# Optimization experiments

Measured on AMD Instinct MI355X. Metric: run time of the kernel, lower is better.

## Reference

```python
import jax, jax.numpy as jnp
import numpy as np

EPS_DIV = 1e-6    # safe_div clamp
EPS_NORM = 1e-12  # F.normalize eps
EPS_PD = 1e-6     # F.pairwise_distance eps (added to the difference)


def setup_inputs() -> dict:
    key = jax.random.key(0)
    k1, k2, k3 = jax.random.split(key, 3)
    B, N, D, C = 8, 2048, 512, 8192
    x = jax.random.normal(k1, (B, N, D), dtype=jnp.float32)
    W = jax.random.normal(k2, (D, D), dtype=jnp.float32) * (1.0 / np.sqrt(D))
    codebook = jax.random.normal(k3, (C, D), dtype=jnp.float32)
    return {"x": x, "W": W, "codebook": codebook}


def reference(x, W, codebook):
    sg = jax.lax.stop_gradient
    # implicit codebook = Linear(dim, dim, bias=False)(codebook)  -> codebook @ W^T
    imp = codebook @ W.T                                  # [C, D]

    lead = x.shape[:-1]
    D = x.shape[-1]
    xf = x.reshape(-1, D)                                 # [T, D]

    # nearest-neighbor search (no_grad in original): squared-dist argmin == cdist argmin
    d2 = (jnp.sum(xf * xf, axis=-1, keepdims=True)
          - 2.0 * (xf @ imp.T)
          + jnp.sum(imp * imp, axis=-1)[None, :])         # [T, C]
    indices = jnp.argmin(sg(d2), axis=-1)                 # [T]

    qf = imp[indices]                                     # [T, D] gather

    # commit loss: (pairwise_distance(x, q.detach())**2).mean(); torch adds eps to the diff
    diff = xf - sg(qf) + EPS_PD
    commit_loss = jnp.mean(jnp.sum(diff * diff, axis=-1))

    # rotation trick
    norm_x = jnp.linalg.norm(xf, axis=-1, keepdims=True)  # [T, 1]
    norm_q = jnp.linalg.norm(qf, axis=-1, keepdims=True)
    u = xf / jnp.maximum(norm_x, EPS_DIV)
    q = qf / jnp.maximum(norm_q, EPS_DIV)
    s = u + q
    w = sg(s / jnp.maximum(jnp.linalg.norm(s, axis=-1, keepdims=True), EPS_NORM))
    e = xf
    # e - 2 (e.w) w + 2 (e.u_sg) q_sg   (rank-1 products per row)
    rot = (e
           - 2.0 * jnp.sum(e * w, axis=-1, keepdims=True) * w
           + 2.0 * jnp.sum(e * sg(u), axis=-1, keepdims=True) * sg(q))
    quantized = rot * sg(norm_q / jnp.maximum(norm_x, EPS_DIV))

    quantized = quantized.reshape(*lead, D)
    indices = indices.reshape(*lead)
    return quantized, indices, commit_loss
```

## Files before the change

### kernel.cpp

```cpp
#include <hip/hip_runtime.h>
#include <cstdint>
#include <cstddef>

#define DD 512
#define TT 16384
#define CC 8192
#define RT 256
#define CT 128
#define NSPLIT (CC / CT)
#define EPS_DIV 1e-6f
#define EPS_NORM 1e-12f
#define EPS_PD 1e-6f

typedef _Float16 half8 __attribute__((ext_vector_type(8)));
typedef _Float16 half4 __attribute__((ext_vector_type(4)));
typedef float floatx4 __attribute__((ext_vector_type(4)));

#define GLDS16(g, l) __builtin_amdgcn_global_load_lds( \
    (const __attribute__((address_space(1))) void*)(g), \
    (__attribute__((address_space(3))) void*)(l), 16, 0, 0)

__global__ __launch_bounds__(256) void k_prep(
    const float* __restrict__ cb, const float* __restrict__ W,
    _Float16* __restrict__ cbs, _Float16* __restrict__ Ws) {
  const int b = blockIdx.x;
  const float* src;
  _Float16* dst;
  int row;
  if (b < CC / 2) {
    row = b * 2 + (threadIdx.x >> 7);
    src = cb; dst = cbs;
  } else {
    row = (b - CC / 2) * 2 + (threadIdx.x >> 7);
    src = W; dst = Ws;
  }
  const int col = (threadIdx.x & 127) * 4;
  float4 v = *(const float4*)(src + (size_t)row * DD + col);
  half4 h, l;
  h.x = (_Float16)v.x; l.x = (_Float16)(v.x - (float)h.x);
  h.y = (_Float16)v.y; l.y = (_Float16)(v.y - (float)h.y);
  h.z = (_Float16)v.z; l.z = (_Float16)(v.z - (float)h.z);
  h.w = (_Float16)v.w; l.w = (_Float16)(v.w - (float)h.w);
  *(half4*)(dst + (size_t)row * 1024 + col) = h;
  *(half4*)(dst + (size_t)row * 1024 + 512 + col) = l;
}

__global__ __launch_bounds__(256) void k_gemm_mfma(
    const _Float16* __restrict__ cbs, const _Float16* __restrict__ Ws,
    float* __restrict__ imp, _Float16* __restrict__ ih,
    float* __restrict__ cnp) {
  __shared__ __align__(16) char smem[65536];
  const int tid = threadIdx.x;
  const int w = tid >> 6, lane = tid & 63;
  const int quad = lane >> 4, l15 = lane & 15;
  const int wm = (w & 1) * 64, wn = (w >> 1) * 64;
  const int c0 = blockIdx.x * 128;
  const int n0 = blockIdx.y * 128;

  const int srow8 = lane >> 3;
  const int scol = ((lane & 7) ^ srow8) << 3;
  size_t arow[4], brow[4];
#pragma unroll
  for (int j = 0; j < 4; ++j) {
    arow[j] = (size_t)(c0 + j * 32 + w * 8 + srow8) * 1024 + scol;
    brow[j] = (size_t)(n0 + j * 32 + w * 8 + srow8) * 1024 + scol;
  }
  int aoff[4], boff[4];
#pragma unroll
  for (int i = 0; i < 4; ++i) {
    aoff[i] = ((wm + i * 16 + l15) * 64 + ((quad ^ (l15 & 7)) << 3)) * 2;
    boff[i] = ((wn + i * 16 + l15) * 64 + ((quad ^ (l15 & 7)) << 3)) * 2;
  }

  auto stage = [&](int buf, int ak, int bk) {
    char* ab = smem + buf * 32768;
    char* bb = ab + 16384;
#pragma unroll
    for (int j = 0; j < 4; ++j) {
      GLDS16(cbs + arow[j] + ak, (_Float16*)ab + (j * 32 + w * 8) * 64);
      GLDS16(Ws  + brow[j] + bk, (_Float16*)bb + (j * 32 + w * 8) * 64);
    }
  };

  floatx4 acc[4][4] = {};
  stage(0, 0, 0);
#pragma unroll 2
  for (int it = 0; it < 24; ++it) {
    __syncthreads();
    if (it < 23) {
      const int n = it + 1;
      const int p = n >> 3, kk = n & 7;
      const int ak = ((p == 2) ? 512 : 0) + kk * 64;
      const int bk = ((p == 1) ? 512 : 0) + kk * 64;
      stage(n & 1, ak, bk);
    }
    const char* ab = smem + (it & 1) * 32768;
    const char* bb = ab + 16384;
#pragma unroll
    for (int ks = 0; ks < 2; ++ks) {
      const int kx = ks * 64;
      half8 a[4], b[4];
#pragma unroll
      for (int mi = 0; mi < 4; ++mi)
        a[mi] = *(const half8*)(ab + (aoff[mi] ^ kx));
#pragma unroll
      for (int ni = 0; ni < 4; ++ni)
        b[ni] = *(const half8*)(bb + (boff[ni] ^ kx));
#pragma unroll
      for (int mi = 0; mi < 4; ++mi)
#pragma unroll
        for (int ni = 0; ni < 4; ++ni)
          acc[mi][ni] = __builtin_amdgcn_mfma_f32_16x16x32_f16(
              a[mi], b[ni], acc[mi][ni], 0, 0, 0);
    }
  }
  __syncthreads();
  float* Csh = (float*)smem;
#pragma unroll
  for (int mi = 0; mi < 4; ++mi)
#pragma unroll
    for (int r = 0; r < 4; ++r) {
      const int row = wm + mi * 16 + quad * 4 + r;
      const int key = (row & 7) << 2;
#pragma unroll
      for (int ni = 0; ni < 4; ++ni) {
        const int col = wn + ni * 16 + l15;
        Csh[row * 128 + (col ^ key)] = acc[mi][ni][r];
      }
    }
  __syncthreads();
#pragma unroll
  for (int i = 0; i < 16; ++i) {
    const int row = (tid >> 5) * 16 + i;
    const int col = (tid & 31) * 4;
    const int key = (row & 7) << 2;
    const float4 v = *(const float4*)&Csh[row * 128 + (col ^ key)];
    *(float4*)&imp[(size_t)(c0 + row) * DD + n0 + col] = v;
    half4 h;
    h.x = (_Float16)v.x; h.y = (_Float16)v.y;
    h.z = (_Float16)v.z; h.w = (_Float16)v.w;
    *(half4*)&ih[(size_t)(c0 + row) * DD + n0 + col] = h;
    float ss = v.x * v.x + v.y * v.y + v.z * v.z + v.w * v.w;
#pragma unroll
    for (int m = 1; m < 32; m <<= 1) ss += __shfl_xor(ss, m);
    if ((tid & 31) == 0) cnp[(size_t)(n0 >> 7) * CC + c0 + row] = ss;
  }
}

__global__ __launch_bounds__(256) void k_cast_cnorm(
    const float* __restrict__ x, _Float16* __restrict__ xh,
    const float* __restrict__ cnp, float* __restrict__ cnorm) {
  const int b = blockIdx.x;
  if (b < TT / 2) {
    const size_t base = (size_t)b * 1024 + threadIdx.x * 4;
    float4 v = *(const float4*)(x + base);
    half4 h;
    h.x = (_Float16)v.x; h.y = (_Float16)v.y;
    h.z = (_Float16)v.z; h.w = (_Float16)v.w;
    *(half4*)(xh + base) = h;
  } else {
    const int row = (b - TT / 2) * 256 + threadIdx.x;
    cnorm[row] = cnp[row] + cnp[CC + row] + cnp[2 * CC + row] + cnp[3 * CC + row];
  }
}

__global__ __launch_bounds__(256, 2) void k_dist_top2(
    const _Float16* __restrict__ xh, const _Float16* __restrict__ ih,
    const float* __restrict__ cnorm,
    float* __restrict__ bval, int* __restrict__ bidx) {
  __shared__ __align__(16) char smem[49152];
  const int tid = threadIdx.x;
  const int mw = tid >> 6, lane = tid & 63;
  const int quad = lane >> 4, l15 = lane & 15;
  const int r0 = blockIdx.x * RT;
  const int c0 = blockIdx.y * CT;

  const _Float16* gA = xh + (size_t)(r0 + tid) * DD;
  const _Float16* gB = ih + (size_t)(c0 + (tid & 127)) * DD + (tid >> 7) * 8;

  int aoff[4], boff[8];
#pragma unroll
  for (int mi = 0; mi < 4; ++mi)
    aoff[mi] = quad * 4096 + (mw * 64 + mi * 16 + l15) * 16;
#pragma unroll
  for (int ni = 0; ni < 8; ++ni)
    boff[ni] = quad * 2048 + (ni * 16 + l15) * 16;

  auto stage = [&](int s) {
    char* ab = smem + (s & 1) * 24576;
    char* bb = ab + 16384;
    const int k0 = s * 32;
#pragma unroll
    for (int r = 0; r < 4; ++r)
      GLDS16(gA + k0 + r * 8, ab + (r * 256 + mw * 64) * 16);
#pragma unroll
    for (int r = 0; r < 2; ++r)
      GLDS16(gB + k0 + r * 16, bb + (r * 256 + mw * 64) * 16);
  };

  floatx4 acc[4][8] = {};
  stage(0);
#pragma unroll 2
  for (int s = 0; s < 16; ++s) {
    __syncthreads();
    if (s < 15) stage(s + 1);
    const char* ab = smem + (s & 1) * 24576;
    const char* bb = ab + 16384;
    half8 a[4], b[8];
#pragma unroll
    for (int mi = 0; mi < 4; ++mi) a[mi] = *(const half8*)(ab + aoff[mi]);
#pragma unroll
    for (int ni = 0; ni < 8; ++ni) b[ni] = *(const half8*)(bb + boff[ni]);
#pragma unroll
    for (int mi = 0; mi < 4; ++mi)
#pragma unroll
      for (int ni = 0; ni < 8; ++ni)
        acc[mi][ni] = __builtin_amdgcn_mfma_f32_16x16x32_f16(
            a[mi], b[ni], acc[mi][ni], 0, 0, 0);
  }
  float cn[8];
#pragma unroll
  for (int ni = 0; ni < 8; ++ni) cn[ni] = cnorm[c0 + ni * 16 + l15];
  float best[16];
  int bsti[16];
#pragma unroll
  for (int mi = 0; mi < 4; ++mi)
#pragma unroll
    for (int r = 0; r < 4; ++r) {
      const int sl = mi * 4 + r;
      best[sl] = 3.4e38f; bsti[sl] = 0;
#pragma unroll
      for (int ni = 0; ni < 8; ++ni) {
        const float v = fmaf(-2.0f, acc[mi][ni][r], cn[ni]);
        if (v < best[sl]) { best[sl] = v; bsti[sl] = c0 + ni * 16 + l15; }
      }
    }
  __syncthreads();
  float* rv = (float*)smem;
  int* ri = (int*)(smem + 16384);
#pragma unroll
  for (int mi = 0; mi < 4; ++mi)
#pragma unroll
    for (int r = 0; r < 4; ++r) {
      const int rowl = mw * 64 + mi * 16 + quad * 4 + r;
      rv[rowl * 16 + l15] = best[mi * 4 + r];
      ri[rowl * 16 + l15] = bsti[mi * 4 + r];
    }
  __syncthreads();
  {
    const int row = tid;
    float v1 = 3.4e38f, v2 = 3.4e38f;
    int i1 = 0x7fffffff, i2 = 0x7fffffff;
#pragma unroll
    for (int t = 0; t < 16; ++t) {
      const float v = rv[row * 16 + t];
      const int i = ri[row * 16 + t];
      if (v < v1 || (v == v1 && i < i1)) {
        v2 = v1; i2 = i1; v1 = v; i1 = i;
      } else if (v < v2 || (v == v2 && i < i2)) {
        v2 = v; i2 = i;
      }
    }
    const size_t o = ((size_t)blockIdx.y * TT + r0 + row) * 2;
    bval[o] = v1; bval[o + 1] = v2;
    bidx[o] = i1; bidx[o + 1] = i2;
  }
}

__global__ __launch_bounds__(256) void k_epilogue(
    const float* __restrict__ x, const float* __restrict__ imp,
    const float* __restrict__ cnorm,
    const float* __restrict__ bval, const int* __restrict__ bidx,
    float* __restrict__ outq, float* __restrict__ outidx,
    float* __restrict__ rloss) {
  const int lane = threadIdx.x & 63;
  const int row = blockIdx.x * 4 + (threadIdx.x >> 6);
  const size_t o = ((size_t)lane * TT + row) * 2;
  float v1 = bval[o], v2 = bval[o + 1];
  int i1 = bidx[o], i2 = bidx[o + 1];
#pragma unroll
  for (int m = 1; m < 64; m <<= 1) {
    const float w1 = __shfl_xor(v1, m), w2 = __shfl_xor(v2, m);
    const int j1 = __shfl_xor(i1, m), j2 = __shfl_xor(i2, m);
    if (w1 < v1 || (w1 == v1 && j1 < i1)) {
      if (v1 < w2 || (v1 == w2 && i1 < j2)) { v2 = v1; i2 = i1; }
      else { v2 = w2; i2 = j2; }
      v1 = w1; i1 = j1;
    } else {
      if (w1 < v2 || (w1 == v2 && j1 < i2)) { v2 = w1; i2 = j1; }
    }
  }
  const float* xr = x + (size_t)row * DD + lane * 8;
  float e[8], qa[8], qb[8];
  *(float4*)&e[0] = *(const float4*)xr;
  *(float4*)&e[4] = *(const float4*)(xr + 4);
  const float* q1p = imp + (size_t)i1 * DD + lane * 8;
  const float* q2p = imp + (size_t)i2 * DD + lane * 8;
  *(float4*)&qa[0] = *(const float4*)q1p;
  *(float4*)&qa[4] = *(const float4*)(q1p + 4);
  *(float4*)&qb[0] = *(const float4*)q2p;
  *(float4*)&qb[4] = *(const float4*)(q2p + 4);
  float d1 = 0.f, d2 = 0.f;
#pragma unroll
  for (int k = 0; k < 8; ++k) {
    d1 = fmaf(e[k], qa[k], d1);
    d2 = fmaf(e[k], qb[k], d2);
  }
#pragma unroll
  for (int m = 1; m < 64; m <<= 1) {
    d1 += __shfl_xor(d1, m);
    d2 += __shfl_xor(d2, m);
  }
  const float s1 = fmaf(-2.0f, d1, cnorm[i1]);
  const float s2 = fmaf(-2.0f, d2, cnorm[i2]);
  const bool use2 = (s2 < s1) || (s2 == s1 && i2 < i1);
  const int idx = use2 ? i2 : i1;
  float q[8];
#pragma unroll
  for (int k = 0; k < 8; ++k) q[k] = use2 ? qb[k] : qa[k];

  float xx = 0.f, qq = 0.f, xq = 0.f, cl = 0.f;
#pragma unroll
  for (int k = 0; k < 8; ++k) {
    xx = fmaf(e[k], e[k], xx);
    qq = fmaf(q[k], q[k], qq);
    xq = fmaf(e[k], q[k], xq);
    float d = e[k] - q[k] + EPS_PD;
    cl = fmaf(d, d, cl);
  }
#pragma unroll
  for (int m = 1; m < 64; m <<= 1) {
    xx += __shfl_xor(xx, m);
    qq += __shfl_xor(qq, m);
    xq += __shfl_xor(xq, m);
    cl += __shfl_xor(cl, m);
  }
  const float nx = sqrtf(xx), nq = sqrtf(qq);
  const float dx = fmaxf(nx, EPS_DIV), dq = fmaxf(nq, EPS_DIV);
  const float uu = xx / (dx * dx);
  const float qq2 = qq / (dq * dq);
  const float uq = xq / (dx * dq);
  const float ss = uu + qq2 + 2.0f * uq;
  const float dn = fmaxf(sqrtf(ss), EPS_NORM);
  const float es = xx / dx + xq / dq;
  const float a = 2.0f * es / (dn * dn);
  const float b = 2.0f * (xx / dx);
  const float scale = nq / dx;

  float ov[8];
#pragma unroll
  for (int k = 0; k < 8; ++k) {
    const float qp = q[k] / dq;
    const float sk = e[k] / dx + qp;
    ov[k] = (e[k] - a * sk + b * qp) * scale;
  }
  float* op = outq + (size_t)row * DD + lane * 8;
  *(float4*)op = *(const float4*)&ov[0];
  *(float4*)(op + 4) = *(const float4*)&ov[4];
  if (lane == 0) {
    outidx[row] = (float)idx;
    rloss[row] = cl;
  }
}

__global__ __launch_bounds__(256) void k_loss_final(
    const float* __restrict__ rloss, float* __restrict__ out) {
  __shared__ double red[256];
  const int tid = threadIdx.x;
  double s = 0.0;
  for (int i = tid; i < TT; i += 256) s += (double)rloss[i];
  red[tid] = s;
  __syncthreads();
  for (int st = 128; st > 0; st >>= 1) {
    if (tid < st) red[tid] += red[tid + st];
    __syncthreads();
  }
  if (tid == 0) out[0] = (float)(red[0] / (double)TT);
}

extern "C" void kernel_launch(void* const* d_in, const int* in_sizes, int n_in,
                              void* d_out, int out_size, void* d_ws, size_t ws_size,
                              hipStream_t stream) {
  const float* x  = (const float*)d_in[0];
  const float* W  = (const float*)d_in[1];
  const float* cb = (const float*)d_in[2];
  float* out = (float*)d_out;

  float* imp = (float*)d_ws;
  _Float16* ih = (_Float16*)(imp + (size_t)CC * DD);
  _Float16* cbs = ih + (size_t)CC * DD;
  _Float16* xh = cbs;
  _Float16* Ws = cbs + (size_t)CC * 1024;
  float* cnp   = (float*)(Ws + (size_t)DD * 1024);
  float* cnorm = cnp + 4 * CC;
  float* bval  = cnorm + CC;
  int*   bidx  = (int*)(bval + (size_t)NSPLIT * TT * 2);
  float* rloss = (float*)(bidx + (size_t)NSPLIT * TT * 2);

  float* out_q    = out;
  float* out_idx  = out + (size_t)TT * DD;
  float* out_loss = out_idx + TT;

  k_prep<<<CC / 2 + DD / 2, 256, 0, stream>>>(cb, W, cbs, Ws);
  k_gemm_mfma<<<dim3(CC / 128, DD / 128), 256, 0, stream>>>(cbs, Ws, imp, ih, cnp);
  k_cast_cnorm<<<TT / 2 + CC / 256, 256, 0, stream>>>(x, xh, cnp, cnorm);
  k_dist_top2<<<dim3(TT / RT, CC / CT), 256, 0, stream>>>(xh, ih, cnorm, bval, bidx);
  k_epilogue<<<TT / 4, 256, 0, stream>>>(x, imp, cnorm, bval, bidx, out_q, out_idx, rloss);
  k_loss_final<<<1, 256, 0, stream>>>(rloss, out_loss);
}
```

Baseline: 390.5 us.

## Use K-panel layout for fp16 operands and load MFMA fragments directly from global

```diff
diff --git a/kernel.cpp b/kernel.cpp
--- a/kernel.cpp
+++ b/kernel.cpp
@@ -22,32 +22,46 @@
 
 __global__ __launch_bounds__(256) void k_prep(
     const float* __restrict__ cb, const float* __restrict__ W,
-    _Float16* __restrict__ cbs, _Float16* __restrict__ Ws) {
+    const float* __restrict__ x,
+    _Float16* __restrict__ cbs, _Float16* __restrict__ Ws,
+    _Float16* __restrict__ xh_t) {
   const int b = blockIdx.x;
-  const float* src;
-  _Float16* dst;
-  int row;
-  if (b < CC / 2) {
-    row = b * 2 + (threadIdx.x >> 7);
-    src = cb; dst = cbs;
+  if (b < CC / 2 + DD / 2) {
+    const float* src;
+    _Float16* dst;
+    int row;
+    if (b < CC / 2) {
+      row = b * 2 + (threadIdx.x >> 7);
+      src = cb; dst = cbs;
+    } else {
+      row = (b - CC / 2) * 2 + (threadIdx.x >> 7);
+      src = W; dst = Ws;
+    }
+    const int col = (threadIdx.x & 127) * 4;
+    float4 v = *(const float4*)(src + (size_t)row * DD + col);
+    half4 h, l;
+    h.x = (_Float16)v.x; l.x = (_Float16)(v.x - (float)h.x);
+    h.y = (_Float16)v.y; l.y = (_Float16)(v.y - (float)h.y);
+    h.z = (_Float16)v.z; l.z = (_Float16)(v.z - (float)h.z);
+    h.w = (_Float16)v.w; l.w = (_Float16)(v.w - (float)h.w);
+    *(half4*)(dst + (size_t)row * 1024 + col) = h;
+    *(half4*)(dst + (size_t)row * 1024 + 512 + col) = l;
   } else {
-    row = (b - CC / 2) * 2 + (threadIdx.x >> 7);
-    src = W; dst = Ws;
-  }
-  const int col = (threadIdx.x & 127) * 4;
-  float4 v = *(const float4*)(src + (size_t)row * DD + col);
-  half4 h, l;
-  h.x = (_Float16)v.x; l.x = (_Float16)(v.x - (float)h.x);
-  h.y = (_Float16)v.y; l.y = (_Float16)(v.y - (float)h.y);
-  h.z = (_Float16)v.z; l.z = (_Float16)(v.z - (float)h.z);
-  h.w = (_Float16)v.w; l.w = (_Float16)(v.w - (float)h.w);
-  *(half4*)(dst + (size_t)row * 1024 + col) = h;
-  *(half4*)(dst + (size_t)row * 1024 + 512 + col) = l;
+    const int b2 = b - (CC / 2 + DD / 2);
+    const int row = b2 * 2 + (threadIdx.x >> 7);
+    const int col = (threadIdx.x & 127) * 4;
+    float4 v = *(const float4*)(x + (size_t)row * DD + col);
+    half4 h;
+    h.x = (_Float16)v.x; h.y = (_Float16)v.y;
+    h.z = (_Float16)v.z; h.w = (_Float16)v.w;
+    const int p = col >> 5, off = col & 31;
+    *(half4*)(xh_t + ((size_t)p * TT + row) * 32 + off) = h;
+  }
 }
 
 __global__ __launch_bounds__(256) void k_gemm_mfma(
     const _Float16* __restrict__ cbs, const _Float16* __restrict__ Ws,
-    float* __restrict__ imp, _Float16* __restrict__ ih,
+    float* __restrict__ imp, _Float16* __restrict__ ih_t,
     float* __restrict__ cnp) {
   __shared__ __align__(16) char smem[65536];
   const int tid = threadIdx.x;
@@ -139,7 +153,9 @@
     half4 h;
     h.x = (_Float16)v.x; h.y = (_Float16)v.y;
     h.z = (_Float16)v.z; h.w = (_Float16)v.w;
-    *(half4*)&ih[(size_t)(c0 + row) * DD + n0 + col] = h;
+    const int d = n0 + col;
+    const int p = d >> 5, off = d & 31;
+    *(half4*)(ih_t + ((size_t)p * CC + c0 + row) * 32 + off) = h;
     float ss = v.x * v.x + v.y * v.y + v.z * v.z + v.w * v.w;
 #pragma unroll
     for (int m = 1; m < 32; m <<= 1) ss += __shfl_xor(ss, m);
@@ -147,70 +163,38 @@
   }
 }
 
-__global__ __launch_bounds__(256) void k_cast_cnorm(
-    const float* __restrict__ x, _Float16* __restrict__ xh,
-    const float* __restrict__ cnp, float* __restrict__ cnorm) {
-  const int b = blockIdx.x;
-  if (b < TT / 2) {
-    const size_t base = (size_t)b * 1024 + threadIdx.x * 4;
-    float4 v = *(const float4*)(x + base);
-    half4 h;
-    h.x = (_Float16)v.x; h.y = (_Float16)v.y;
-    h.z = (_Float16)v.z; h.w = (_Float16)v.w;
-    *(half4*)(xh + base) = h;
-  } else {
-    const int row = (b - TT / 2) * 256 + threadIdx.x;
-    cnorm[row] = cnp[row] + cnp[CC + row] + cnp[2 * CC + row] + cnp[3 * CC + row];
-  }
-}
-
 __global__ __launch_bounds__(256, 2) void k_dist_top2(
-    const _Float16* __restrict__ xh, const _Float16* __restrict__ ih,
-    const float* __restrict__ cnorm,
+    const _Float16* __restrict__ xh_t, const _Float16* __restrict__ ih_t,
+    const float* __restrict__ cnp,
     float* __restrict__ bval, int* __restrict__ bidx) {
-  __shared__ __align__(16) char smem[49152];
+  __shared__ float rv[256 * 16];
+  __shared__ int   ri[256 * 16];
   const int tid = threadIdx.x;
   const int mw = tid >> 6, lane = tid & 63;
   const int quad = lane >> 4, l15 = lane & 15;
   const int r0 = blockIdx.x * RT;
   const int c0 = blockIdx.y * CT;
 
-  const _Float16* gA = xh + (size_t)(r0 + tid) * DD;
-  const _Float16* gB = ih + (size_t)(c0 + (tid & 127)) * DD + (tid >> 7) * 8;
-
-  int aoff[4], boff[8];
+  const char* pa = (const char*)xh_t;
+  const char* pb = (const char*)ih_t;
+  int voa[4], vob[8];
 #pragma unroll
   for (int mi = 0; mi < 4; ++mi)
-    aoff[mi] = quad * 4096 + (mw * 64 + mi * 16 + l15) * 16;
+    voa[mi] = ((r0 + mw * 64 + mi * 16 + l15) * 32 + quad * 8) * 2;
 #pragma unroll
   for (int ni = 0; ni < 8; ++ni)
-    boff[ni] = quad * 2048 + (ni * 16 + l15) * 16;
-
-  auto stage = [&](int s) {
-    char* ab = smem + (s & 1) * 24576;
-    char* bb = ab + 16384;
-    const int k0 = s * 32;
-#pragma unroll
-    for (int r = 0; r < 4; ++r)
-      GLDS16(gA + k0 + r * 8, ab + (r * 256 + mw * 64) * 16);
-#pragma unroll
-    for (int r = 0; r < 2; ++r)
-      GLDS16(gB + k0 + r * 16, bb + (r * 256 + mw * 64) * 16);
-  };
+    vob[ni] = ((c0 + ni * 16 + l15) * 32 + quad * 8) * 2;
 
   floatx4 acc[4][8] = {};
-  stage(0);
 #pragma unroll 2
   for (int s = 0; s < 16; ++s) {
-    __syncthreads();
-    if (s < 15) stage(s + 1);
-    const char* ab = smem + (s & 1) * 24576;
-    const char* bb = ab + 16384;
+    const char* sa = pa + (size_t)s * (TT * 64);
+    const char* sb = pb + (size_t)s * (CC * 64);
     half8 a[4], b[8];
 #pragma unroll
-    for (int mi = 0; mi < 4; ++mi) a[mi] = *(const half8*)(ab + aoff[mi]);
-#pragma unroll
-    for (int ni = 0; ni < 8; ++ni) b[ni] = *(const half8*)(bb + boff[ni]);
+    for (int mi = 0; mi < 4; ++mi) a[mi] = *(const half8*)(sa + voa[mi]);
+#pragma unroll
+    for (int ni = 0; ni < 8; ++ni) b[ni] = *(const half8*)(sb + vob[ni]);
 #pragma unroll
     for (int mi = 0; mi < 4; ++mi)
 #pragma unroll
@@ -220,7 +204,10 @@
   }
   float cn[8];
 #pragma unroll
-  for (int ni = 0; ni < 8; ++ni) cn[ni] = cnorm[c0 + ni * 16 + l15];
+  for (int ni = 0; ni < 8; ++ni) {
+    const int c = c0 + ni * 16 + l15;
+    cn[ni] = cnp[c] + cnp[CC + c] + cnp[2 * CC + c] + cnp[3 * CC + c];
+  }
   float best[16];
   int bsti[16];
 #pragma unroll
@@ -236,8 +223,6 @@
       }
     }
   __syncthreads();
-  float* rv = (float*)smem;
-  int* ri = (int*)(smem + 16384);
 #pragma unroll
   for (int mi = 0; mi < 4; ++mi)
 #pragma unroll
@@ -269,7 +254,7 @@
 
 __global__ __launch_bounds__(256) void k_epilogue(
     const float* __restrict__ x, const float* __restrict__ imp,
-    const float* __restrict__ cnorm,
+    const float* __restrict__ cnp,
     const float* __restrict__ bval, const int* __restrict__ bidx,
     float* __restrict__ outq, float* __restrict__ outidx,
     float* __restrict__ rloss) {
@@ -311,8 +296,10 @@
     d1 += __shfl_xor(d1, m);
     d2 += __shfl_xor(d2, m);
   }
-  const float s1 = fmaf(-2.0f, d1, cnorm[i1]);
-  const float s2 = fmaf(-2.0f, d2, cnorm[i2]);
+  const float n1 = cnp[i1] + cnp[CC + i1] + cnp[2 * CC + i1] + cnp[3 * CC + i1];
+  const float n2 = cnp[i2] + cnp[CC + i2] + cnp[2 * CC + i2] + cnp[3 * CC + i2];
+  const float s1 = fmaf(-2.0f, d1, n1);
+  const float s2 = fmaf(-2.0f, d2, n2);
   const bool use2 = (s2 < s1) || (s2 == s1 && i2 < i1);
   const int idx = use2 ? i2 : i1;
   float q[8];
@@ -387,24 +374,22 @@
   float* out = (float*)d_out;
 
   float* imp = (float*)d_ws;
-  _Float16* ih = (_Float16*)(imp + (size_t)CC * DD);
-  _Float16* cbs = ih + (size_t)CC * DD;
-  _Float16* xh = cbs;
-  _Float16* Ws = cbs + (size_t)CC * 1024;
+  _Float16* ih_t = (_Float16*)(imp + (size_t)CC * DD);
+  _Float16* xh_t = ih_t + (size_t)CC * DD;
+  _Float16* Ws = xh_t + (size_t)TT * DD;
   float* cnp   = (float*)(Ws + (size_t)DD * 1024);
-  float* cnorm = cnp + 4 * CC;
-  float* bval  = cnorm + CC;
+  float* rloss = cnp + 4 * CC;
+  _Float16* cbs = (_Float16*)(rloss + TT);
+  float* bval  = (float*)cbs;
   int*   bidx  = (int*)(bval + (size_t)NSPLIT * TT * 2);
-  float* rloss = (float*)(bidx + (size_t)NSPLIT * TT * 2);
 
   float* out_q    = out;
   float* out_idx  = out + (size_t)TT * DD;
   float* out_loss = out_idx + TT;
 
-  k_prep<<<CC / 2 + DD / 2, 256, 0, stream>>>(cb, W, cbs, Ws);
-  k_gemm_mfma<<<dim3(CC / 128, DD / 128), 256, 0, stream>>>(cbs, Ws, imp, ih, cnp);
-  k_cast_cnorm<<<TT / 2 + CC / 256, 256, 0, stream>>>(x, xh, cnp, cnorm);
-  k_dist_top2<<<dim3(TT / RT, CC / CT), 256, 0, stream>>>(xh, ih, cnorm, bval, bidx);
-  k_epilogue<<<TT / 4, 256, 0, stream>>>(x, imp, cnorm, bval, bidx, out_q, out_idx, rloss);
+  k_prep<<<CC / 2 + DD / 2 + TT / 2, 256, 0, stream>>>(cb, W, x, cbs, Ws, xh_t);
+  k_gemm_mfma<<<dim3(CC / 128, DD / 128), 256, 0, stream>>>(cbs, Ws, imp, ih_t, cnp);
+  k_dist_top2<<<dim3(TT / RT, CC / CT), 256, 0, stream>>>(xh_t, ih_t, cnp, bval, bidx);
+  k_epilogue<<<TT / 4, 256, 0, stream>>>(x, imp, cnp, bval, bidx, out_q, out_idx, rloss);
   k_loss_final<<<1, 256, 0, stream>>>(rloss, out_loss);
 }
```

Result: faster. 373.3 us (-4.4%).
